# Kernel tuning notes

Hardware: AMD Instinct MI355X
Metric: run time of the kernel (lower is better)

Reference implementation:

```python
import jax, jax.numpy as jnp
import numpy as np
from jax import lax

EPS = 1e-5  # nn.InstanceNorm2d default
DN = ('NCHW', 'OIHW', 'NCHW')


def conv2d(x, w, b, pad):
    y = lax.conv_general_dilated(x, w, window_strides=(1, 1),
                                 padding=((pad, pad), (pad, pad)),
                                 dimension_numbers=DN)
    return y + b[None, :, None, None]


def instance_norm(x):
    # per-(N,C) normalization over H,W; affine=False (InstanceNorm2d default)
    mu = jnp.mean(x, axis=(2, 3), keepdims=True)
    var = jnp.var(x, axis=(2, 3), keepdims=True)
    return (x - mu) * lax.rsqrt(var + EPS)


def maxpool2(x):
    return lax.reduce_window(x, -jnp.inf, lax.max,
                             (1, 1, 2, 2), (1, 1, 2, 2), 'VALID')


def setup_inputs() -> dict:
    key = jax.random.key(0)
    ks = jax.random.split(key, 12)
    B = 2048
    x = jax.random.normal(ks[0], (B, 1, 28, 28), dtype=jnp.float32)
    def w(k, shape, fan_in):
        return jax.random.normal(k, shape, dtype=jnp.float32) * (1.0 / np.sqrt(fan_in))
    return {
        'x': x,
        'w1': w(ks[1], (32, 1, 3, 3), 9), 'b1': jnp.zeros((32,), jnp.float32),
        'w2': w(ks[2], (64, 32, 3, 3), 32 * 9), 'b2': jnp.zeros((64,), jnp.float32),
        'w3': w(ks[3], (64, 64, 3, 3), 64 * 9), 'b3': jnp.zeros((64,), jnp.float32),
        'fw1': w(ks[4], (128, 14 * 14 * 64), 14 * 14 * 64), 'fb1': jnp.zeros((128,), jnp.float32),
        'fw2': w(ks[5], (10, 128), 128), 'fb2': jnp.zeros((10,), jnp.float32),
    }


def reference(x, w1, b1, w2, b2, w3, b3, fw1, fb1, fw2, fb2):
    # net1: conv -> IN -> relu -> conv -> IN -> conv -> relu -> maxpool(2)
    h = jax.nn.relu(instance_norm(conv2d(x, w1, b1, 1)))
    h = instance_norm(conv2d(h, w2, b2, 1))
    h = jax.nn.relu(conv2d(h, w3, b3, 1))
    h = maxpool2(h)                       # (B, 64, 14, 14)
    h = h.reshape(h.shape[0], -1)          # flatten C,H,W
    # dropout layers are identity at inference
    h = jax.nn.relu(h @ fw1.T + fb1)
    logits = h @ fw2.T + fb2
    return jax.nn.log_softmax(logits, axis=1)
```

## Files before the change

### kernel.cpp

```cpp
#include <hip/hip_runtime.h>
#include <hip/hip_bf16.h>

typedef unsigned int u32;
typedef _Float16 h2 __attribute__((ext_vector_type(2)));
typedef _Float16 f16x8 __attribute__((ext_vector_type(8)));
typedef float f32x4 __attribute__((ext_vector_type(4)));
typedef u32 u32x4 __attribute__((ext_vector_type(4)));

__device__ __forceinline__ u32 pk(float a, float b) {
    return __builtin_bit_cast(u32, __builtin_amdgcn_cvt_pkrtz(a, b));
}
__device__ __forceinline__ float lo16(u32 v) { h2 h = __builtin_bit_cast(h2, v); return (float)h[0]; }
__device__ __forceinline__ float hi16(u32 v) { h2 h = __builtin_bit_cast(h2, v); return (float)h[1]; }

#define A1O   0
#define A2O   12544
#define STO   37648
#define SB2O  37776
#define SB3O  37840
#define SMEMSZ 37904

__global__ __launch_bounds__(256) void k_pack(const float* __restrict__ w2,
                                              const float* __restrict__ w3,
                                              const float* __restrict__ fw1,
                                              u32* wA2, u32* wA3, u32* wp1) {
    int i = blockIdx.x * 256 + threadIdx.x;
    const int n1 = 9216, n2 = 18432, n3 = 128 * 6272;
    if (i < n1) {
        int r = i & 3, l = (i >> 2) & 63, t2 = i >> 8;
        int ks = t2 % 9, mt = t2 / 9;
        int oc = mt * 16 + (l & 15);
        int ic = (l >> 4) * 8 + 2 * r;
        wA2[i] = pk(w2[(oc * 32 + ic) * 9 + ks], w2[(oc * 32 + ic + 1) * 9 + ks]);
    } else if (i < n1 + n2) {
        int j = i - n1;
        int r = j & 3, l = (j >> 2) & 63, t2 = j >> 8;
        int ks = t2 % 18, mt = t2 / 18;
        int oc = mt * 16 + (l & 15);
        int ic = (ks & 1) * 32 + (l >> 4) * 8 + 2 * r;
        int tap = ks >> 1;
        wA3[j] = pk(w3[(oc * 64 + ic) * 9 + tap], w3[(oc * 64 + ic + 1) * 9 + tap]);
    } else if (i < n1 + n2 + n3) {
        int j = i - n1 - n2;
        int row = j / 6272, u = j % 6272;
        wp1[j] = pk(fw1[row * 12544 + 2 * u], fw1[row * 12544 + 2 * u + 1]);
    }
}

__global__ __launch_bounds__(1024) void k_net(const float* __restrict__ x,
                                              const float* __restrict__ w1,
                                              const float* __restrict__ b1,
                                              const u32* __restrict__ wA2,
                                              const float* __restrict__ b2,
                                              const u32* __restrict__ wA3,
                                              const float* __restrict__ b3,
                                              u32* __restrict__ pflat) {
    __shared__ u32 smem[SMEMSZ];
    u32* a1 = smem + A1O;
    u32* a2 = smem + A2O;
    float* st  = (float*)(smem + STO);
    float* sb2 = (float*)(smem + SB2O);
    float* sb3 = (float*)(smem + SB3O);
    float* xs  = (float*)(smem + A1O);
    float* c1f = (float*)(smem + A2O);

    const int b = blockIdx.x, t = threadIdx.x;
    const int wv = t >> 6, l = t & 63;
    const int xi = l & 15, kg = l >> 4;

    if (t < 64) { sb2[t] = b2[t]; sb3[t] = b3[t]; }
    for (int i = t; i < 900; i += 1024) xs[i] = 0.f;
    __syncthreads();
    const float* xb = x + b * 784;
    for (int i = t; i < 784; i += 1024) xs[(i / 28 + 1) * 30 + (i % 28) + 1] = xb[i];
    __syncthreads();
    for (int i = t; i < 25088; i += 1024) {
        int oc = i / 784, p = i - oc * 784;
        const float* base = &xs[(p / 28) * 30 + (p % 28)];
        float acc = b1[oc];
        const float* w = &w1[oc * 9];
#pragma unroll
        for (int r = 0; r < 3; ++r)
#pragma unroll
            for (int c = 0; c < 3; ++c) acc += base[r * 30 + c] * w[3 * r + c];
        c1f[i] = acc;
    }
    __syncthreads();
    for (int oc = wv; oc < 32; oc += 16) {
        float s = 0.f, s2 = 0.f;
        for (int p = l; p < 784; p += 64) { float v = c1f[oc * 784 + p]; s += v; s2 += v * v; }
#pragma unroll
        for (int off = 32; off; off >>= 1) { s += __shfl_xor(s, off); s2 += __shfl_xor(s2, off); }
        if (l == 0) {
            float mu = s * (1.f / 784.f);
            float var = s2 * (1.f / 784.f) - mu * mu;
            st[2 * oc] = mu; st[2 * oc + 1] = rsqrtf(var + 1e-5f);
        }
    }
    __syncthreads();
    for (int i = t; i < 12544; i += 1024) {
        int cp = i / 784, p = i - cp * 784;
        float f0 = (c1f[(2 * cp) * 784 + p]     - st[4 * cp])     * st[4 * cp + 1];
        float f1 = (c1f[(2 * cp + 1) * 784 + p] - st[4 * cp + 2]) * st[4 * cp + 3];
        a1[p * 16 + (cp ^ (((p >> 1) & 3) << 2))] = pk(fmaxf(f0, 0.f), fmaxf(f1, 0.f));
    }
    __syncthreads();

    for (int j = 0; j < 4; ++j) {
        int nt = wv + 16 * j;
        if (nt >= 56) break;
        int y = nt >> 1, hs = nt & 1;
        f32x4 acc[4];
#pragma unroll
        for (int mt = 0; mt < 4; ++mt)
#pragma unroll
            for (int r = 0; r < 4; ++r) acc[mt][r] = sb2[mt * 16 + kg * 4 + r];
#pragma unroll 2
        for (int ks = 0; ks < 9; ++ks) {
            int dy = ks / 3, dx = ks % 3;
            int yy = y + dy - 1;
            if ((unsigned)yy >= 28u) continue;
            int xx = hs * 16 + xi + dx - 1;
            int ax = xx < 0 ? 0 : (xx > 27 ? 27 : xx);
            int pp = yy * 28 + ax;
            u32x4 bv = *(const u32x4*)&a1[pp * 16 + ((kg * 4) ^ (((pp >> 1) & 3) << 2))];
            u32x4 z = {0u, 0u, 0u, 0u};
            bv = ((unsigned)xx < 28u) ? bv : z;
#pragma unroll
            for (int mt = 0; mt < 4; ++mt) {
                u32x4 av = *(const u32x4*)(wA2 + (((mt * 9 + ks) * 64 + l) << 2));
                acc[mt] = __builtin_amdgcn_mfma_f32_16x16x32_f16(
                    __builtin_bit_cast(f16x8, av),
                    __builtin_bit_cast(f16x8, bv), acc[mt], 0, 0, 0);
            }
        }
        int xx = hs * 16 + xi;
        if (xx < 28) {
            int p = y * 28 + xx;
            int sw = (p & 7) << 2;
#pragma unroll
            for (int mt = 0; mt < 4; ++mt) {
                int cp0 = mt * 8 + kg * 2;
                a2[p * 32 + (cp0 ^ sw)]       = pk(acc[mt][0], acc[mt][1]);
                a2[p * 32 + ((cp0 + 1) ^ sw)] = pk(acc[mt][2], acc[mt][3]);
            }
        }
    }
    __syncthreads();
    for (int ch = wv; ch < 64; ch += 16) {
        float s = 0.f, s2 = 0.f;
        int cp = ch >> 1, hi = ch & 1;
        for (int p = l; p < 784; p += 64) {
            u32 v = a2[p * 32 + (cp ^ ((p & 7) << 2))];
            float f = hi ? hi16(v) : lo16(v);
            s += f; s2 += f * f;
        }
#pragma unroll
        for (int off = 32; off; off >>= 1) { s += __shfl_xor(s, off); s2 += __shfl_xor(s2, off); }
        if (l == 0) {
            float mu = s * (1.f / 784.f);
            float var = s2 * (1.f / 784.f) - mu * mu;
            st[2 * ch] = mu; st[2 * ch + 1] = rsqrtf(var + 1e-5f);
        }
    }
    __syncthreads();
    for (int i = t; i < 25088; i += 1024) {
        int p = i >> 5, cp = i & 31;
        int idx = p * 32 + (cp ^ ((p & 7) << 2));
        u32 v = a2[idx];
        a2[idx] = pk((lo16(v) - st[4 * cp]) * st[4 * cp + 1],
                     (hi16(v) - st[4 * cp + 2]) * st[4 * cp + 3]);
    }
    __syncthreads();

    {
        unsigned short* dstp = (unsigned short*)pflat;
        for (int j = 0; j < 4; ++j) {
            int nt = wv + 16 * j;
            if (nt >= 56) break;
            int pr = nt >> 1, mh = nt & 1;
            int r2 = pr >> 1, hh = pr & 1;
            f32x4 acc[2][2];
#pragma unroll
            for (int sub = 0; sub < 2; ++sub)
#pragma unroll
                for (int mtl = 0; mtl < 2; ++mtl)
#pragma unroll
                    for (int rr = 0; rr < 4; ++rr)
                        acc[sub][mtl][rr] = sb3[(mh * 2 + mtl) * 16 + kg * 4 + rr];
#pragma unroll 2
            for (int ks = 0; ks < 18; ++ks) {
                int tap = ks >> 1, kh = ks & 1;
                int dy = tap / 3, dx = tap % 3;
                int xx = hh * 16 + xi + dx - 1;
                int ax = xx < 0 ? 0 : (xx > 27 ? 27 : xx);
                bool mk = (unsigned)xx < 28u;
                u32x4 av[2];
#pragma unroll
                for (int mtl = 0; mtl < 2; ++mtl)
                    av[mtl] = *(const u32x4*)(wA3 + ((((mh * 2 + mtl) * 18 + ks) * 64 + l) << 2));
#pragma unroll
                for (int sub = 0; sub < 2; ++sub) {
                    int yy = 2 * r2 + sub + dy - 1;
                    if ((unsigned)yy >= 28u) continue;
                    int pp = yy * 28 + ax;
                    u32x4 bv = *(const u32x4*)&a2[pp * 32 + ((kh * 16 + kg * 4) ^ ((pp & 7) << 2))];
                    u32x4 z = {0u, 0u, 0u, 0u};
                    bv = mk ? bv : z;
#pragma unroll
                    for (int mtl = 0; mtl < 2; ++mtl)
                        acc[sub][mtl] = __builtin_amdgcn_mfma_f32_16x16x32_f16(
                            __builtin_bit_cast(f16x8, av[mtl]),
                            __builtin_bit_cast(f16x8, bv), acc[sub][mtl], 0, 0, 0);
                }
            }
#pragma unroll
            for (int mtl = 0; mtl < 2; ++mtl)
#pragma unroll
                for (int rr = 0; rr < 4; ++rr) {
                    float v = fmaxf(acc[0][mtl][rr], acc[1][mtl][rr]);
                    v = fmaxf(v, 0.f);
                    float partner = __shfl_xor(v, 1);
                    float hx = fmaxf(v, partner);
                    int xx = hh * 16 + xi;
                    if ((xi & 1) == 0 && xx < 28) {
                        int px = xx >> 1;
                        int oc = (mh * 2 + mtl) * 16 + kg * 4 + rr;
                        dstp[b * 12544 + oc * 196 + r2 * 14 + px] =
                            __builtin_bit_cast(unsigned short, (_Float16)hx);
                    }
                }
        }
    }
}

__global__ __launch_bounds__(512) void k_fc(const u32* __restrict__ pflat,
                                            const u32* __restrict__ wp1,
                                            const float* __restrict__ fb1,
                                            const float* __restrict__ fw2,
                                            const float* __restrict__ fb2,
                                            float* __restrict__ out) {
    __shared__ float ph[8 * 128 * 16];
    __shared__ float hbuf[16 * 129];
    __shared__ float lg[160];
    const int t = threadIdx.x, wv = t >> 6, l = t & 63;
    const int xi = l & 15, kg = l >> 4;
    const int img0 = blockIdx.x * 16;

    f32x4 acc[8];
#pragma unroll
    for (int mt = 0; mt < 8; ++mt)
#pragma unroll
        for (int r = 0; r < 4; ++r) acc[mt][r] = 0.f;

    const u32* bbase = pflat + (size_t)(img0 + xi) * 6272;
#pragma unroll 2
    for (int kk = 0; kk < 49; ++kk) {
        int koff = (wv * 49 + kk) * 16 + kg * 4;
        u32x4 bv = *(const u32x4*)(bbase + koff);
#pragma unroll
        for (int mt = 0; mt < 8; ++mt) {
            u32x4 av = *(const u32x4*)(wp1 + (size_t)(mt * 16 + xi) * 6272 + koff);
            acc[mt] = __builtin_amdgcn_mfma_f32_16x16x32_f16(
                __builtin_bit_cast(f16x8, av),
                __builtin_bit_cast(f16x8, bv), acc[mt], 0, 0, 0);
        }
    }
#pragma unroll
    for (int mt = 0; mt < 8; ++mt)
#pragma unroll
        for (int r = 0; r < 4; ++r)
            ph[(wv * 128 + mt * 16 + kg * 4 + r) * 16 + xi] = acc[mt][r];
    __syncthreads();
    for (int i = t; i < 2048; i += 512) {
        int o = i >> 4, img = i & 15;
        float s = fb1[o];
#pragma unroll
        for (int w = 0; w < 8; ++w) s += ph[(w * 128 + o) * 16 + img];
        hbuf[img * 129 + o] = s > 0.f ? s : 0.f;
    }
    __syncthreads();
    if (t < 160) {
        int img = t / 10, c = t % 10;
        float s = fb2[c];
        for (int j = 0; j < 128; ++j) s += hbuf[img * 129 + j] * fw2[c * 128 + j];
        lg[t] = s;
    }
    __syncthreads();
    if (t < 16) {
        float m = -1e30f;
        for (int c = 0; c < 10; ++c) m = fmaxf(m, lg[t * 10 + c]);
        float s = 0.f;
        for (int c = 0; c < 10; ++c) s += expf(lg[t * 10 + c] - m);
        float ls = logf(s);
        for (int c = 0; c < 10; ++c)
            out[(img0 + t) * 10 + c] = lg[t * 10 + c] - m - ls;
    }
}

extern "C" void kernel_launch(void* const* d_in, const int* in_sizes, int n_in,
                              void* d_out, int out_size, void* d_ws, size_t ws_size,
                              hipStream_t stream) {
    const float* x   = (const float*)d_in[0];
    const float* w1  = (const float*)d_in[1];
    const float* b1  = (const float*)d_in[2];
    const float* w2  = (const float*)d_in[3];
    const float* b2  = (const float*)d_in[4];
    const float* w3  = (const float*)d_in[5];
    const float* b3  = (const float*)d_in[6];
    const float* fw1 = (const float*)d_in[7];
    const float* fb1 = (const float*)d_in[8];
    const float* fw2 = (const float*)d_in[9];
    const float* fb2 = (const float*)d_in[10];
    float* out = (float*)d_out;

    const size_t PFL = (size_t)2048 * 6272;
    const size_t WA2 = 9216, WA3 = 18432, WP1 = (size_t)128 * 6272;

    u32* ws = (u32*)d_ws;
    u32* pflat = ws;
    u32* wA2   = pflat + PFL;
    u32* wA3   = wA2 + WA2;
    u32* wp1   = wA3 + WA3;

    const int n_pack = (int)(WA2 + WA3 + WP1);
    k_pack<<<(n_pack + 255) / 256, 256, 0, stream>>>(w2, w3, fw1, wA2, wA3, wp1);
    k_net<<<2048, 1024, 0, stream>>>(x, w1, b1, wA2, b2, wA3, b3, pflat);
    k_fc<<<128, 512, 0, stream>>>(pflat, wp1, fb1, fw2, fb2, out);
}
```

Baseline: 646.0 us.

## Fuse conv1 into packed layout, pair-channel norm stats, reuse rows in conv3, halve FC tile

Conv1 now computes all 32 channels per pixel from register-held taps and writes packed fp16 straight into the swizzled a1 layout. This removes the fp32 staging buffer and its extra LDS pass. Both instance-norm stat passes now handle two channels per wave from packed data, and the normalize loops load per-thread channel constants once. Conv3 loads four input rows once per dx/kh and reuses them across the three dy taps and both pooled rows, with all four output tiles per wave. The FC kernel processes 8 images per block across 256 blocks for more parallelism, at the cost of half the MFMA lanes being redundant.

```diff
diff --git a/kernel.cpp b/kernel.cpp
--- a/kernel.cpp
+++ b/kernel.cpp
@@ -61,8 +61,7 @@
     float* st  = (float*)(smem + STO);
     float* sb2 = (float*)(smem + SB2O);
     float* sb3 = (float*)(smem + SB3O);
-    float* xs  = (float*)(smem + A1O);
-    float* c1f = (float*)(smem + A2O);
+    float* xs  = (float*)(smem + A2O);
 
     const int b = blockIdx.x, t = threadIdx.x;
     const int wv = t >> 6, l = t & 63;
@@ -74,35 +73,58 @@
     const float* xb = x + b * 784;
     for (int i = t; i < 784; i += 1024) xs[(i / 28 + 1) * 30 + (i % 28) + 1] = xb[i];
     __syncthreads();
-    for (int i = t; i < 25088; i += 1024) {
-        int oc = i / 784, p = i - oc * 784;
+    if (t < 784) {
+        int p = t;
         const float* base = &xs[(p / 28) * 30 + (p % 28)];
-        float acc = b1[oc];
-        const float* w = &w1[oc * 9];
+        float rx[9];
 #pragma unroll
         for (int r = 0; r < 3; ++r)
 #pragma unroll
-            for (int c = 0; c < 3; ++c) acc += base[r * 30 + c] * w[3 * r + c];
-        c1f[i] = acc;
-    }
-    __syncthreads();
-    for (int oc = wv; oc < 32; oc += 16) {
-        float s = 0.f, s2 = 0.f;
-        for (int p = l; p < 784; p += 64) { float v = c1f[oc * 784 + p]; s += v; s2 += v * v; }
-#pragma unroll
-        for (int off = 32; off; off >>= 1) { s += __shfl_xor(s, off); s2 += __shfl_xor(s2, off); }
+            for (int c = 0; c < 3; ++c) rx[r * 3 + c] = base[r * 30 + c];
+        int sw = ((p >> 1) & 3) << 2;
+#pragma unroll 4
+        for (int cp = 0; cp < 16; ++cp) {
+            float s0 = b1[2 * cp], s1 = b1[2 * cp + 1];
+#pragma unroll
+            for (int k = 0; k < 9; ++k) {
+                s0 += rx[k] * w1[(2 * cp) * 9 + k];
+                s1 += rx[k] * w1[(2 * cp + 1) * 9 + k];
+            }
+            a1[p * 16 + (cp ^ sw)] = pk(s0, s1);
+        }
+    }
+    __syncthreads();
+    {
+        int cp = wv;
+        float s0 = 0.f, q0 = 0.f, s1 = 0.f, q1 = 0.f;
+        for (int p = l; p < 784; p += 64) {
+            u32 v = a1[p * 16 + (cp ^ (((p >> 1) & 3) << 2))];
+            float f0 = lo16(v), f1 = hi16(v);
+            s0 += f0; q0 += f0 * f0; s1 += f1; q1 += f1 * f1;
+        }
+#pragma unroll
+        for (int off = 32; off; off >>= 1) {
+            s0 += __shfl_xor(s0, off); q0 += __shfl_xor(q0, off);
+            s1 += __shfl_xor(s1, off); q1 += __shfl_xor(q1, off);
+        }
         if (l == 0) {
-            float mu = s * (1.f / 784.f);
-            float var = s2 * (1.f / 784.f) - mu * mu;
-            st[2 * oc] = mu; st[2 * oc + 1] = rsqrtf(var + 1e-5f);
-        }
-    }
-    __syncthreads();
-    for (int i = t; i < 12544; i += 1024) {
-        int cp = i / 784, p = i - cp * 784;
-        float f0 = (c1f[(2 * cp) * 784 + p]     - st[4 * cp])     * st[4 * cp + 1];
-        float f1 = (c1f[(2 * cp + 1) * 784 + p] - st[4 * cp + 2]) * st[4 * cp + 3];
-        a1[p * 16 + (cp ^ (((p >> 1) & 3) << 2))] = pk(fmaxf(f0, 0.f), fmaxf(f1, 0.f));
+            float mu0 = s0 * (1.f / 784.f), mu1 = s1 * (1.f / 784.f);
+            st[4 * cp + 0] = mu0;
+            st[4 * cp + 1] = rsqrtf(q0 * (1.f / 784.f) - mu0 * mu0 + 1e-5f);
+            st[4 * cp + 2] = mu1;
+            st[4 * cp + 3] = rsqrtf(q1 * (1.f / 784.f) - mu1 * mu1 + 1e-5f);
+        }
+    }
+    __syncthreads();
+    {
+        int cp = (t & 15) ^ (((t >> 5) & 3) << 2);
+        float mu0 = st[4 * cp], ri0 = st[4 * cp + 1];
+        float mu1 = st[4 * cp + 2], ri1 = st[4 * cp + 3];
+        for (int i = t; i < 12544; i += 1024) {
+            u32 v = a1[i];
+            a1[i] = pk(fmaxf((lo16(v) - mu0) * ri0, 0.f),
+                       fmaxf((hi16(v) - mu1) * ri1, 0.f));
+        }
     }
     __syncthreads();
 
@@ -147,75 +169,89 @@
         }
     }
     __syncthreads();
-    for (int ch = wv; ch < 64; ch += 16) {
-        float s = 0.f, s2 = 0.f;
-        int cp = ch >> 1, hi = ch & 1;
+    for (int cp = wv; cp < 32; cp += 16) {
+        float s0 = 0.f, q0 = 0.f, s1 = 0.f, q1 = 0.f;
         for (int p = l; p < 784; p += 64) {
             u32 v = a2[p * 32 + (cp ^ ((p & 7) << 2))];
-            float f = hi ? hi16(v) : lo16(v);
-            s += f; s2 += f * f;
-        }
-#pragma unroll
-        for (int off = 32; off; off >>= 1) { s += __shfl_xor(s, off); s2 += __shfl_xor(s2, off); }
+            float f0 = lo16(v), f1 = hi16(v);
+            s0 += f0; q0 += f0 * f0; s1 += f1; q1 += f1 * f1;
+        }
+#pragma unroll
+        for (int off = 32; off; off >>= 1) {
+            s0 += __shfl_xor(s0, off); q0 += __shfl_xor(q0, off);
+            s1 += __shfl_xor(s1, off); q1 += __shfl_xor(q1, off);
+        }
         if (l == 0) {
-            float mu = s * (1.f / 784.f);
-            float var = s2 * (1.f / 784.f) - mu * mu;
-            st[2 * ch] = mu; st[2 * ch + 1] = rsqrtf(var + 1e-5f);
-        }
-    }
-    __syncthreads();
-    for (int i = t; i < 25088; i += 1024) {
-        int p = i >> 5, cp = i & 31;
-        int idx = p * 32 + (cp ^ ((p & 7) << 2));
-        u32 v = a2[idx];
-        a2[idx] = pk((lo16(v) - st[4 * cp]) * st[4 * cp + 1],
-                     (hi16(v) - st[4 * cp + 2]) * st[4 * cp + 3]);
+            float mu0 = s0 * (1.f / 784.f), mu1 = s1 * (1.f / 784.f);
+            st[4 * cp + 0] = mu0;
+            st[4 * cp + 1] = rsqrtf(q0 * (1.f / 784.f) - mu0 * mu0 + 1e-5f);
+            st[4 * cp + 2] = mu1;
+            st[4 * cp + 3] = rsqrtf(q1 * (1.f / 784.f) - mu1 * mu1 + 1e-5f);
+        }
+    }
+    __syncthreads();
+    {
+        int cp = (t & 31) ^ (((t >> 5) & 7) << 2);
+        float mu0 = st[4 * cp], ri0 = st[4 * cp + 1];
+        float mu1 = st[4 * cp + 2], ri1 = st[4 * cp + 3];
+        for (int i = t; i < 25088; i += 1024) {
+            u32 v = a2[i];
+            a2[i] = pk((lo16(v) - mu0) * ri0, (hi16(v) - mu1) * ri1);
+        }
     }
     __syncthreads();
 
     {
         unsigned short* dstp = (unsigned short*)pflat;
-        for (int j = 0; j < 4; ++j) {
-            int nt = wv + 16 * j;
-            if (nt >= 56) break;
-            int pr = nt >> 1, mh = nt & 1;
-            int r2 = pr >> 1, hh = pr & 1;
-            f32x4 acc[2][2];
+        for (int j = 0; j < 2; ++j) {
+            int u = wv + 16 * j;
+            if (u >= 28) break;
+            int r2 = u >> 1, hh = u & 1;
+            f32x4 acc[2][4];
 #pragma unroll
             for (int sub = 0; sub < 2; ++sub)
 #pragma unroll
-                for (int mtl = 0; mtl < 2; ++mtl)
+                for (int mtl = 0; mtl < 4; ++mtl)
 #pragma unroll
                     for (int rr = 0; rr < 4; ++rr)
-                        acc[sub][mtl][rr] = sb3[(mh * 2 + mtl) * 16 + kg * 4 + rr];
-#pragma unroll 2
-            for (int ks = 0; ks < 18; ++ks) {
-                int tap = ks >> 1, kh = ks & 1;
-                int dy = tap / 3, dx = tap % 3;
+                        acc[sub][mtl][rr] = sb3[mtl * 16 + kg * 4 + rr];
+#pragma unroll 1
+            for (int dx = 0; dx < 3; ++dx) {
                 int xx = hh * 16 + xi + dx - 1;
                 int ax = xx < 0 ? 0 : (xx > 27 ? 27 : xx);
                 bool mk = (unsigned)xx < 28u;
-                u32x4 av[2];
-#pragma unroll
-                for (int mtl = 0; mtl < 2; ++mtl)
-                    av[mtl] = *(const u32x4*)(wA3 + ((((mh * 2 + mtl) * 18 + ks) * 64 + l) << 2));
-#pragma unroll
-                for (int sub = 0; sub < 2; ++sub) {
-                    int yy = 2 * r2 + sub + dy - 1;
-                    if ((unsigned)yy >= 28u) continue;
-                    int pp = yy * 28 + ax;
-                    u32x4 bv = *(const u32x4*)&a2[pp * 32 + ((kh * 16 + kg * 4) ^ ((pp & 7) << 2))];
-                    u32x4 z = {0u, 0u, 0u, 0u};
-                    bv = mk ? bv : z;
-#pragma unroll
-                    for (int mtl = 0; mtl < 2; ++mtl)
-                        acc[sub][mtl] = __builtin_amdgcn_mfma_f32_16x16x32_f16(
-                            __builtin_bit_cast(f16x8, av[mtl]),
-                            __builtin_bit_cast(f16x8, bv), acc[sub][mtl], 0, 0, 0);
+#pragma unroll
+                for (int kh = 0; kh < 2; ++kh) {
+                    u32x4 bvr[4];
+#pragma unroll
+                    for (int rr = 0; rr < 4; ++rr) {
+                        int yy = 2 * r2 - 1 + rr;
+                        u32x4 z = {0u, 0u, 0u, 0u};
+                        bvr[rr] = z;
+                        if (((unsigned)yy < 28u) && mk) {
+                            int pp = yy * 28 + ax;
+                            bvr[rr] = *(const u32x4*)&a2[pp * 32 +
+                                        ((kh * 16 + kg * 4) ^ ((pp & 7) << 2))];
+                        }
+                    }
+#pragma unroll
+                    for (int dy = 0; dy < 3; ++dy) {
+                        int ks = (dy * 3 + dx) * 2 + kh;
+#pragma unroll
+                        for (int mtl = 0; mtl < 4; ++mtl) {
+                            u32x4 av = *(const u32x4*)(wA3 + (((mtl * 18 + ks) * 64 + l) << 2));
+                            acc[0][mtl] = __builtin_amdgcn_mfma_f32_16x16x32_f16(
+                                __builtin_bit_cast(f16x8, av),
+                                __builtin_bit_cast(f16x8, bvr[dy]), acc[0][mtl], 0, 0, 0);
+                            acc[1][mtl] = __builtin_amdgcn_mfma_f32_16x16x32_f16(
+                                __builtin_bit_cast(f16x8, av),
+                                __builtin_bit_cast(f16x8, bvr[dy + 1]), acc[1][mtl], 0, 0, 0);
+                        }
+                    }
                 }
             }
 #pragma unroll
-            for (int mtl = 0; mtl < 2; ++mtl)
+            for (int mtl = 0; mtl < 4; ++mtl)
 #pragma unroll
                 for (int rr = 0; rr < 4; ++rr) {
                     float v = fmaxf(acc[0][mtl][rr], acc[1][mtl][rr]);
@@ -225,7 +261,7 @@
                     int xx = hh * 16 + xi;
                     if ((xi & 1) == 0 && xx < 28) {
                         int px = xx >> 1;
-                        int oc = (mh * 2 + mtl) * 16 + kg * 4 + rr;
+                        int oc = mtl * 16 + kg * 4 + rr;
                         dstp[b * 12544 + oc * 196 + r2 * 14 + px] =
                             __builtin_bit_cast(unsigned short, (_Float16)hx);
                     }
@@ -240,12 +276,12 @@
                                             const float* __restrict__ fw2,
                                             const float* __restrict__ fb2,
                                             float* __restrict__ out) {
-    __shared__ float ph[8 * 128 * 16];
-    __shared__ float hbuf[16 * 129];
-    __shared__ float lg[160];
+    __shared__ float ph[8 * 128 * 8];
+    __shared__ float hbuf[8 * 129];
+    __shared__ float lg[80];
     const int t = threadIdx.x, wv = t >> 6, l = t & 63;
     const int xi = l & 15, kg = l >> 4;
-    const int img0 = blockIdx.x * 16;
+    const int img0 = blockIdx.x * 8;
 
     f32x4 acc[8];
 #pragma unroll
@@ -253,7 +289,7 @@
 #pragma unroll
         for (int r = 0; r < 4; ++r) acc[mt][r] = 0.f;
 
-    const u32* bbase = pflat + (size_t)(img0 + xi) * 6272;
+    const u32* bbase = pflat + (size_t)(img0 + (xi & 7)) * 6272;
 #pragma unroll 2
     for (int kk = 0; kk < 49; ++kk) {
         int koff = (wv * 49 + kk) * 16 + kg * 4;
@@ -266,28 +302,30 @@
                 __builtin_bit_cast(f16x8, bv), acc[mt], 0, 0, 0);
         }
     }
-#pragma unroll
-    for (int mt = 0; mt < 8; ++mt)
-#pragma unroll
-        for (int r = 0; r < 4; ++r)
-            ph[(wv * 128 + mt * 16 + kg * 4 + r) * 16 + xi] = acc[mt][r];
-    __syncthreads();
-    for (int i = t; i < 2048; i += 512) {
-        int o = i >> 4, img = i & 15;
+    if (xi < 8) {
+#pragma unroll
+        for (int mt = 0; mt < 8; ++mt)
+#pragma unroll
+            for (int r = 0; r < 4; ++r)
+                ph[(wv * 128 + mt * 16 + kg * 4 + r) * 8 + xi] = acc[mt][r];
+    }
+    __syncthreads();
+    for (int i = t; i < 1024; i += 512) {
+        int o = i >> 3, img = i & 7;
         float s = fb1[o];
 #pragma unroll
-        for (int w = 0; w < 8; ++w) s += ph[(w * 128 + o) * 16 + img];
+        for (int w = 0; w < 8; ++w) s += ph[(w * 128 + o) * 8 + img];
         hbuf[img * 129 + o] = s > 0.f ? s : 0.f;
     }
     __syncthreads();
-    if (t < 160) {
+    if (t < 80) {
         int img = t / 10, c = t % 10;
         float s = fb2[c];
         for (int j = 0; j < 128; ++j) s += hbuf[img * 129 + j] * fw2[c * 128 + j];
         lg[t] = s;
     }
     __syncthreads();
-    if (t < 16) {
+    if (t < 8) {
         float m = -1e30f;
         for (int c = 0; c < 10; ++c) m = fmaxf(m, lg[t * 10 + c]);
         float s = 0.f;
@@ -326,5 +364,5 @@
     const int n_pack = (int)(WA2 + WA3 + WP1);
     k_pack<<<(n_pack + 255) / 256, 256, 0, stream>>>(w2, w3, fw1, wA2, wA3, wp1);
     k_net<<<2048, 1024, 0, stream>>>(x, w1, b1, wA2, b2, wA3, b3, pflat);
-    k_fc<<<128, 512, 0, stream>>>(pflat, wp1, fb1, fw2, fb2, out);
-}
+    k_fc<<<256, 512, 0, stream>>>(pflat, wp1, fb1, fw2, fb2, out);
+}
```

Result: faster. 587.7 us (-9.0%).
